# Performance work log

Hardware: AMD Instinct MI355X
Metric: run time of the kernel (lower is better)

## Reference

```python
import jax, jax.numpy as jnp
import numpy as np

B, T, D, H = 64, 1024, 300, 512
Hd = H // 2  # per-direction GRU hidden size


def setup_inputs() -> dict:
    key = jax.random.key(0)
    ks = jax.random.split(key, 12)
    s = 0.05
    return {
        "x": jax.random.normal(ks[0], (B, T, D), jnp.float32),
        "lengths": jax.random.randint(ks[1], (B,), 1, T + 1, jnp.int32),
        # forward-direction GRU params (torch layout: [3*Hd, in])
        "w_ih_f": jax.random.normal(ks[2], (3 * Hd, D), jnp.float32) * s,
        "w_hh_f": jax.random.normal(ks[3], (3 * Hd, Hd), jnp.float32) * s,
        "b_ih_f": jax.random.normal(ks[4], (3 * Hd,), jnp.float32) * s,
        "b_hh_f": jax.random.normal(ks[5], (3 * Hd,), jnp.float32) * s,
        # backward-direction GRU params
        "w_ih_b": jax.random.normal(ks[6], (3 * Hd, D), jnp.float32) * s,
        "w_hh_b": jax.random.normal(ks[7], (3 * Hd, Hd), jnp.float32) * s,
        "b_ih_b": jax.random.normal(ks[8], (3 * Hd,), jnp.float32) * s,
        "b_hh_b": jax.random.normal(ks[9], (3 * Hd,), jnp.float32) * s,
        # attention: hidden layer [H, H] + bias, context vector [H] (no bias)
        "att_w": jax.random.normal(ks[10], (H, H), jnp.float32) * s,
        "att_b": jnp.zeros((H,), jnp.float32),
        "ctx_v": jax.random.normal(ks[11], (H,), jnp.float32) * s,
    }


def _gru_dir(x, w_ih, w_hh, b_ih, b_hh):
    """Single-direction GRU over padded [B,T,D] input, h0=0. Torch gate math."""
    gx = jnp.einsum("btd,gd->btg", x, w_ih) + b_ih  # [B,T,3Hd], big GEMM up front

    def step(h, gx_t):
        gh = h @ w_hh.T + b_hh
        xr, xz, xn = jnp.split(gx_t, 3, axis=-1)
        hr, hz, hn = jnp.split(gh, 3, axis=-1)
        r = jax.nn.sigmoid(xr + hr)
        z = jax.nn.sigmoid(xz + hz)
        n = jnp.tanh(xn + r * hn)
        h = (1.0 - z) * n + z * h
        return h, h

    h0 = jnp.zeros((x.shape[0], w_hh.shape[1]), x.dtype)
    _, hs = jax.lax.scan(step, h0, jnp.swapaxes(gx, 0, 1))  # [T,B,Hd]
    return jnp.swapaxes(hs, 0, 1)  # [B,T,Hd]


def _forward(x, lengths, w_ih_f, w_hh_f, b_ih_f, b_hh_f,
             w_ih_b, w_hh_b, b_ih_b, b_hh_b, att_w, att_b, ctx_v):
    mask = jnp.arange(T)[None, :] < lengths[:, None]  # [B,T]
    xm = x * mask[..., None].astype(x.dtype)  # original pads sequences with 0
    # bidirectional GRU: backward dir runs over the full padded sequence
    # (zeros included), exactly like the original padded nn.GRU call.
    enc_f = _gru_dir(xm, w_ih_f, w_hh_f, b_ih_f, b_hh_f)
    enc_b = _gru_dir(xm[:, ::-1], w_ih_b, w_hh_b, b_ih_b, b_hh_b)[:, ::-1]
    enc = jnp.concatenate([enc_f, enc_b], axis=-1)  # [B,T,H]
    # attention: tanh hidden layer -> context vector -> masked softmax over T
    u = jnp.tanh(jnp.einsum("bth,oh->bto", enc, att_w) + att_b)
    logits = jnp.einsum("bth,h->bt", u, ctx_v)
    logits = jnp.where(mask, logits, -jnp.inf)
    att = jax.nn.softmax(logits, axis=-1)  # pad positions get exact 0 weight
    return jnp.einsum("bt,bth->bh", att, enc)  # weighted sum pooling -> [B,H]


def reference(x, lengths, w_ih_f, w_hh_f, b_ih_f, b_hh_f,
              w_ih_b, w_hh_b, b_ih_b, b_hh_b, att_w, att_b, ctx_v):
    return _forward(x, lengths, w_ih_f, w_hh_f, b_ih_f, b_hh_f,
                    w_ih_b, w_hh_b, b_ih_b, b_hh_b, att_w, att_b, ctx_v)
```

## Files before the change

### kernel.cpp

```cpp
#include <hip/hip_runtime.h>

#define T_SEQ 1024
#define BATCH 64
#define DIN   300
#define DPAD  320
#define HD    256
#define NW    1536
#define ROWS  65536

typedef _Float16 f16x8 __attribute__((ext_vector_type(8)));
typedef _Float16 h2_t  __attribute__((ext_vector_type(2)));
typedef float    f32x4 __attribute__((ext_vector_type(4)));

__device__ __forceinline__ float dot2f(h2_t a, h2_t b, float c) {
#if __has_builtin(__builtin_amdgcn_fdot2)
    return __builtin_amdgcn_fdot2(a, b, c, false);
#else
    return c + (float)a[0]*(float)b[0] + (float)a[1]*(float)b[1];
#endif
}

__device__ __forceinline__ float sigmoidf_(float x) { return 1.f/(1.f+__expf(-x)); }
__device__ __forceinline__ float tanhf_(float x)    { return 1.f - 2.f/(__expf(2.f*x)+1.f); }

__global__ void prep_x(const float* __restrict__ x, const int* __restrict__ len,
                       _Float16* __restrict__ xh) {
    int r = blockIdx.x, k = threadIdx.x;
    int b = r >> 10, t = r & 1023;
    float v = (k < DIN && t < len[b]) ? x[(size_t)r*DIN + k] : 0.f;
    xh[(size_t)r*DPAD + k] = (_Float16)v;
}

__global__ void prep_w(const float* __restrict__ wihf, const float* __restrict__ wihb,
                       const float* __restrict__ bihf, const float* __restrict__ bihb,
                       const float* __restrict__ attw,
                       _Float16* __restrict__ wih, _Float16* __restrict__ attwh,
                       float* __restrict__ bih) {
    int bid = blockIdx.x, tid = threadIdx.x;
    if (bid < NW) {
        const float* src = (bid < 768) ? (wihf + (size_t)bid*DIN)
                                       : (wihb + (size_t)(bid-768)*DIN);
        if (tid < DPAD)
            wih[(size_t)bid*DPAD + tid] = (_Float16)((tid < DIN) ? src[tid] : 0.f);
        if (tid == 0)
            bih[bid] = (bid < 768) ? bihf[bid] : bihb[bid-768];
    } else {
        int n = bid - NW;
        attwh[(size_t)n*512 + tid] = (_Float16)attw[(size_t)n*512 + tid];
    }
}

__global__ __launch_bounds__(256) void gemm_gx(const _Float16* __restrict__ xh,
                                               const _Float16* __restrict__ wih,
                                               const float* __restrict__ bih,
                                               _Float16* __restrict__ gx) {
    int m0 = blockIdx.x * 64, n0 = blockIdx.y * 128;
    __shared__ _Float16 As[64][40];
    __shared__ _Float16 Bs[128][40];
    int tid = threadIdx.x;
    int wave = tid >> 6, lane = tid & 63;
    f32x4 acc[8] = {};
    for (int kt = 0; kt < 10; ++kt) {
        int k0 = kt * 32;
        {
            int r = tid >> 2, ko = (tid & 3) * 8;
            *(f16x8*)&As[r][ko] = *(const f16x8*)&xh[(size_t)(m0+r)*DPAD + k0 + ko];
        }
        {
            int r = tid >> 1, ko = (tid & 1) * 16;
            *(f16x8*)&Bs[r][ko]   = *(const f16x8*)&wih[(size_t)(n0+r)*DPAD + k0 + ko];
            *(f16x8*)&Bs[r][ko+8] = *(const f16x8*)&wih[(size_t)(n0+r)*DPAD + k0 + ko + 8];
        }
        __syncthreads();
        int kk = (lane >> 4) * 8;
        f16x8 a = *(const f16x8*)&As[wave*16 + (lane & 15)][kk];
#pragma unroll
        for (int nf = 0; nf < 8; ++nf) {
            f16x8 bfr = *(const f16x8*)&Bs[nf*16 + (lane & 15)][kk];
            acc[nf] = __builtin_amdgcn_mfma_f32_16x16x32_f16(a, bfr, acc[nf], 0, 0, 0);
        }
        __syncthreads();
    }
#pragma unroll
    for (int nf = 0; nf < 8; ++nf) {
        int n = n0 + nf*16 + (lane & 15);
        float bv = bih[n];
#pragma unroll
        for (int r = 0; r < 4; ++r) {
            int m = m0 + wave*16 + (lane >> 4)*4 + r;
            gx[(size_t)m*NW + n] = (_Float16)(acc[nf][r] + bv);
        }
    }
}

__global__ void __launch_bounds__(512)
__attribute__((amdgpu_waves_per_eu(2, 2)))
gru_kernel(
        const float* __restrict__ whhf, const float* __restrict__ whhb,
        const float* __restrict__ bhhf, const float* __restrict__ bhhb,
        const _Float16* __restrict__ gx, _Float16* __restrict__ enc) {
    int bid = blockIdx.x;
    int dir = bid & 1, b = bid >> 1;
    int tid = threadIdx.x;
    int j = tid >> 1;
    int half = tid & 1;
    const float* whh = dir ? whhb : whhf;
    const float* bhh = dir ? bhhb : bhhf;

    h2_t wr[64], wz[64], wn[64];
    {
        const float2* pr = (const float2*)(whh + (size_t)j*HD        + half*128);
        const float2* pz = (const float2*)(whh + (size_t)(HD + j)*HD + half*128);
        const float2* pn = (const float2*)(whh + (size_t)(2*HD+j)*HD + half*128);
#pragma unroll
        for (int k2 = 0; k2 < 64; ++k2) {
            float2 a = pr[k2]; wr[k2] = h2_t{(_Float16)a.x, (_Float16)a.y};
            float2 c = pz[k2]; wz[k2] = h2_t{(_Float16)c.x, (_Float16)c.y};
            float2 d = pn[k2]; wn[k2] = h2_t{(_Float16)d.x, (_Float16)d.y};
        }
    }
    float brh = half ? 0.f : bhh[j];
    float bzh = half ? 0.f : bhh[HD + j];
    float bnh = half ? 0.f : bhh[2*HD + j];

    __shared__ __align__(16) _Float16 hbuf[2][HD];
    if (tid < HD) hbuf[0][tid] = (_Float16)0.f;
    float hprev = 0.f;
    __syncthreads();

    const _Float16* gxb = gx + (size_t)b*T_SEQ*NW + dir*768 + j;
    int t = dir ? (T_SEQ - 1) : 0;
    int dt = dir ? -1 : 1;
    const _Float16* gp0 = gxb + (size_t)t*NW;
    float xr = (float)gp0[0], xz = (float)gp0[HD], xn = (float)gp0[2*HD];
    int cur = 0;

    for (int s = 0; s < T_SEQ; ++s) {
        float nxr = 0.f, nxz = 0.f, nxn = 0.f;
        if (s + 1 < T_SEQ) {
            const _Float16* gq = gxb + (size_t)(t + dt)*NW;
            nxr = (float)gq[0]; nxz = (float)gq[HD]; nxn = (float)gq[2*HD];
        }

        float hr0 = brh, hz0 = bzh, hn0 = bnh;
        float hr1 = 0.f, hz1 = 0.f, hn1 = 0.f;
        const _Float16* hb = &hbuf[cur][half*128];
#pragma unroll
        for (int k = 0; k < 16; ++k) {
            f16x8 hv = *(const f16x8*)&hb[k*8];
            h2_t a0 = {hv[0], hv[1]}, a1 = {hv[2], hv[3]};
            h2_t a2 = {hv[4], hv[5]}, a3 = {hv[6], hv[7]};
            hr0 = dot2f(a0, wr[4*k+0], hr0); hr1 = dot2f(a1, wr[4*k+1], hr1);
            hr0 = dot2f(a2, wr[4*k+2], hr0); hr1 = dot2f(a3, wr[4*k+3], hr1);
            hz0 = dot2f(a0, wz[4*k+0], hz0); hz1 = dot2f(a1, wz[4*k+1], hz1);
            hz0 = dot2f(a2, wz[4*k+2], hz0); hz1 = dot2f(a3, wz[4*k+3], hz1);
            hn0 = dot2f(a0, wn[4*k+0], hn0); hn1 = dot2f(a1, wn[4*k+1], hn1);
            hn0 = dot2f(a2, wn[4*k+2], hn0); hn1 = dot2f(a3, wn[4*k+3], hn1);
        }
        float hr = hr0 + hr1, hz = hz0 + hz1, hn = hn0 + hn1;
        hr += __shfl_xor(hr, 1);
        hz += __shfl_xor(hz, 1);
        hn += __shfl_xor(hn, 1);

        float r  = sigmoidf_(xr + hr);
        float z  = sigmoidf_(xz + hz);
        float nn = tanhf_(xn + r * hn);
        float h  = (1.f - z) * nn + z * hprev;
        hprev = h;
        float hnb = __shfl_xor(h, 2);
        if (!half)
            enc[((size_t)(b*T_SEQ + t))*512 + dir*HD + j] = (_Float16)h;
        if ((tid & 3) == 0) {
            h2_t hp = {(_Float16)h, (_Float16)hnb};
            *(h2_t*)&hbuf[cur ^ 1][j] = hp;
        }
        __syncthreads();
        xr = nxr; xz = nxz; xn = nxn;
        cur ^= 1; t += dt;
    }
}

__global__ __launch_bounds__(256) void gemm_u(const _Float16* __restrict__ enc,
                                              const _Float16* __restrict__ attwh,
                                              const float* __restrict__ attb,
                                              const float* __restrict__ ctx,
                                              float* __restrict__ logits) {
    int m0 = blockIdx.x * 64;
    __shared__ _Float16 As[64][40];
    __shared__ _Float16 Bs[512][40];
    int tid = threadIdx.x;
    int wave = tid >> 6, lane = tid & 63;
    f32x4 acc[32] = {};
    for (int kt = 0; kt < 16; ++kt) {
        int k0 = kt * 32;
        {
            int r = tid >> 2, ko = (tid & 3) * 8;
            *(f16x8*)&As[r][ko] = *(const f16x8*)&enc[(size_t)(m0+r)*512 + k0 + ko];
        }
        {
#pragma unroll
            for (int jr = 0; jr < 2; ++jr) {
                int row = tid*2 + jr;
#pragma unroll
                for (int q = 0; q < 4; ++q)
                    *(f16x8*)&Bs[row][q*8] =
                        *(const f16x8*)&attwh[(size_t)row*512 + k0 + q*8];
            }
        }
        __syncthreads();
        int kk = (lane >> 4) * 8;
        f16x8 a = *(const f16x8*)&As[wave*16 + (lane & 15)][kk];
#pragma unroll
        for (int nf = 0; nf < 32; ++nf) {
            f16x8 bfr = *(const f16x8*)&Bs[nf*16 + (lane & 15)][kk];
            acc[nf] = __builtin_amdgcn_mfma_f32_16x16x32_f16(a, bfr, acc[nf], 0, 0, 0);
        }
        __syncthreads();
    }
    float rs0 = 0.f, rs1 = 0.f, rs2 = 0.f, rs3 = 0.f;
#pragma unroll
    for (int nf = 0; nf < 32; ++nf) {
        int n = nf*16 + (lane & 15);
        float bv = attb[n], cv = ctx[n];
        rs0 += tanhf_(acc[nf][0] + bv) * cv;
        rs1 += tanhf_(acc[nf][1] + bv) * cv;
        rs2 += tanhf_(acc[nf][2] + bv) * cv;
        rs3 += tanhf_(acc[nf][3] + bv) * cv;
    }
#pragma unroll
    for (int off = 1; off < 16; off <<= 1) {
        rs0 += __shfl_xor(rs0, off);
        rs1 += __shfl_xor(rs1, off);
        rs2 += __shfl_xor(rs2, off);
        rs3 += __shfl_xor(rs3, off);
    }
    if ((lane & 15) == 0) {
        int mb = m0 + wave*16 + (lane >> 4)*4;
        logits[mb + 0] = rs0;
        logits[mb + 1] = rs1;
        logits[mb + 2] = rs2;
        logits[mb + 3] = rs3;
    }
}

__global__ __launch_bounds__(256) void softmax_pool(const float* __restrict__ logits,
                                                    const _Float16* __restrict__ enc,
                                                    const int* __restrict__ lengths,
                                                    float* __restrict__ out) {
    int b = blockIdx.x, tid = threadIdx.x;
    int len = lengths[b];
    if (len < 1) len = 1;
    if (len > T_SEQ) len = T_SEQ;
    __shared__ float att[T_SEQ];
    __shared__ float red[8];
    const float* lg = logits + (size_t)b*T_SEQ;

    float m = -1e30f;
    for (int t = tid; t < len; t += 256) m = fmaxf(m, lg[t]);
#pragma unroll
    for (int off = 1; off < 64; off <<= 1) m = fmaxf(m, __shfl_xor(m, off));
    if ((tid & 63) == 0) red[tid >> 6] = m;
    __syncthreads();
    m = fmaxf(fmaxf(red[0], red[1]), fmaxf(red[2], red[3]));

    float s = 0.f;
    for (int t = tid; t < len; t += 256) {
        float e = __expf(lg[t] - m);
        att[t] = e;
        s += e;
    }
#pragma unroll
    for (int off = 1; off < 64; off <<= 1) s += __shfl_xor(s, off);
    if ((tid & 63) == 0) red[4 + (tid >> 6)] = s;
    __syncthreads();
    s = red[4] + red[5] + red[6] + red[7];
    float inv = 1.f / s;

    float a0 = 0.f, a1 = 0.f;
    const _Float16* eb = enc + (size_t)b*T_SEQ*512;
    for (int t = 0; t < len; ++t) {
        float w = att[t];
        a0 += w * (float)eb[(size_t)t*512 + tid];
        a1 += w * (float)eb[(size_t)t*512 + 256 + tid];
    }
    out[(size_t)b*512 + tid]       = a0 * inv;
    out[(size_t)b*512 + 256 + tid] = a1 * inv;
}

extern "C" void kernel_launch(void* const* d_in, const int* in_sizes, int n_in,
                              void* d_out, int out_size, void* d_ws, size_t ws_size,
                              hipStream_t stream) {
    const float* x    = (const float*)d_in[0];
    const int*   len  = (const int*)  d_in[1];
    const float* wihf = (const float*)d_in[2];
    const float* whhf = (const float*)d_in[3];
    const float* bihf = (const float*)d_in[4];
    const float* bhhf = (const float*)d_in[5];
    const float* wihb = (const float*)d_in[6];
    const float* whhb = (const float*)d_in[7];
    const float* bihb = (const float*)d_in[8];
    const float* bhhb = (const float*)d_in[9];
    const float* attw = (const float*)d_in[10];
    const float* attb = (const float*)d_in[11];
    const float* ctxv = (const float*)d_in[12];
    float* out = (float*)d_out;

    char* ws = (char*)d_ws;
    size_t off = 0;
    _Float16* xh    = (_Float16*)(ws + off); off += (size_t)ROWS*DPAD*2;
    _Float16* wih   = (_Float16*)(ws + off); off += (size_t)NW*DPAD*2;
    _Float16* attwh = (_Float16*)(ws + off); off += (size_t)512*512*2;
    float*    bih   = (float*)   (ws + off); off += (size_t)NW*4;
    _Float16* gx    = (_Float16*)(ws + off); off += (size_t)ROWS*NW*2;
    _Float16* enc   = (_Float16*)(ws + off); off += (size_t)ROWS*512*2;
    float*    logit = (float*)   (ws + off); off += (size_t)ROWS*4;

    prep_x<<<dim3(ROWS), dim3(DPAD), 0, stream>>>(x, len, xh);
    prep_w<<<dim3(NW + 512), dim3(512), 0, stream>>>(wihf, wihb, bihf, bihb, attw,
                                                     wih, attwh, bih);
    gemm_gx<<<dim3(ROWS/64, NW/128), dim3(256), 0, stream>>>(xh, wih, bih, gx);
    gru_kernel<<<dim3(2*BATCH), dim3(512), 0, stream>>>(whhf, whhb, bhhf, bhhb, gx, enc);
    gemm_u<<<dim3(ROWS/64), dim3(256), 0, stream>>>(enc, attwh, attb, ctxv, logit);
    softmax_pool<<<dim3(BATCH), dim3(256), 0, stream>>>(logit, enc, len, out);
}
```

Measured before the change: 1.709 ms.

## Hold z/n recurrent weights in AGPRs and pack encoder output stores

Moves the z and n gate recurrent weight fragments into accumulation registers with inline asm, read back with v_accvgpr_read before each dot2. This relieves VGPR pressure, and the waves_per_eu(2,2) attribute is dropped. The encoder output write is also merged into the same half2 store that updates the shared hidden buffer. The risk is the extra accvgpr_read instructions on the serial per-step critical path.

```diff
diff --git a/kernel.cpp b/kernel.cpp
--- a/kernel.cpp
+++ b/kernel.cpp
@@ -18,6 +18,17 @@
 #else
     return c + (float)a[0]*(float)b[0] + (float)a[1]*(float)b[1];
 #endif
+}
+
+#define AGPR_W(dst, src) \
+    asm volatile("v_accvgpr_write_b32 %0, %1" : "=a"(dst) : "v"(src))
+__device__ __forceinline__ int agpr_r(int a) {
+    int v;
+    asm volatile("v_accvgpr_read_b32 %0, %1" : "=v"(v) : "a"(a));
+    return v;
+}
+__device__ __forceinline__ float dot2a(h2_t h, int wbits, float c) {
+    return dot2f(h, __builtin_bit_cast(h2_t, agpr_r(wbits)), c);
 }
 
 __device__ __forceinline__ float sigmoidf_(float x) { return 1.f/(1.f+__expf(-x)); }
@@ -94,7 +105,6 @@
 }
 
 __global__ void __launch_bounds__(512)
-__attribute__((amdgpu_waves_per_eu(2, 2)))
 gru_kernel(
         const float* __restrict__ whhf, const float* __restrict__ whhb,
         const float* __restrict__ bhhf, const float* __restrict__ bhhb,
@@ -107,16 +117,22 @@
     const float* whh = dir ? whhb : whhf;
     const float* bhh = dir ? bhhb : bhhf;
 
-    h2_t wr[64], wz[64], wn[64];
+    h2_t wr[64];
+    int  wza[64], wna[64];
     {
         const float2* pr = (const float2*)(whh + (size_t)j*HD        + half*128);
         const float2* pz = (const float2*)(whh + (size_t)(HD + j)*HD + half*128);
         const float2* pn = (const float2*)(whh + (size_t)(2*HD+j)*HD + half*128);
 #pragma unroll
-        for (int k2 = 0; k2 < 64; ++k2) {
-            float2 a = pr[k2]; wr[k2] = h2_t{(_Float16)a.x, (_Float16)a.y};
-            float2 c = pz[k2]; wz[k2] = h2_t{(_Float16)c.x, (_Float16)c.y};
-            float2 d = pn[k2]; wn[k2] = h2_t{(_Float16)d.x, (_Float16)d.y};
+        for (int k = 0; k < 64; ++k) {
+            float2 a = pr[k];
+            wr[k] = h2_t{(_Float16)a.x, (_Float16)a.y};
+            float2 c = pz[k];
+            h2_t z2 = h2_t{(_Float16)c.x, (_Float16)c.y};
+            AGPR_W(wza[k], __builtin_bit_cast(int, z2));
+            float2 d = pn[k];
+            h2_t n2 = h2_t{(_Float16)d.x, (_Float16)d.y};
+            AGPR_W(wna[k], __builtin_bit_cast(int, n2));
         }
     }
     float brh = half ? 0.f : bhh[j];
@@ -142,22 +158,22 @@
             nxr = (float)gq[0]; nxz = (float)gq[HD]; nxn = (float)gq[2*HD];
         }
 
-        float hr0 = brh, hz0 = bzh, hn0 = bnh;
-        float hr1 = 0.f, hz1 = 0.f, hn1 = 0.f;
-        const _Float16* hb = &hbuf[cur][half*128];
-#pragma unroll
-        for (int k = 0; k < 16; ++k) {
-            f16x8 hv = *(const f16x8*)&hb[k*8];
+        float ar = brh, az = bzh, an = bnh;
+        float ar1 = 0.f, az1 = 0.f, an1 = 0.f;
+        const _Float16* hseg = &hbuf[cur][half*128];
+#pragma unroll
+        for (int k8 = 0; k8 < 16; ++k8) {
+            f16x8 hv = *(const f16x8*)&hseg[k8*8];
             h2_t a0 = {hv[0], hv[1]}, a1 = {hv[2], hv[3]};
             h2_t a2 = {hv[4], hv[5]}, a3 = {hv[6], hv[7]};
-            hr0 = dot2f(a0, wr[4*k+0], hr0); hr1 = dot2f(a1, wr[4*k+1], hr1);
-            hr0 = dot2f(a2, wr[4*k+2], hr0); hr1 = dot2f(a3, wr[4*k+3], hr1);
-            hz0 = dot2f(a0, wz[4*k+0], hz0); hz1 = dot2f(a1, wz[4*k+1], hz1);
-            hz0 = dot2f(a2, wz[4*k+2], hz0); hz1 = dot2f(a3, wz[4*k+3], hz1);
-            hn0 = dot2f(a0, wn[4*k+0], hn0); hn1 = dot2f(a1, wn[4*k+1], hn1);
-            hn0 = dot2f(a2, wn[4*k+2], hn0); hn1 = dot2f(a3, wn[4*k+3], hn1);
-        }
-        float hr = hr0 + hr1, hz = hz0 + hz1, hn = hn0 + hn1;
+            ar  = dot2f(a0, wr[4*k8+0], ar);  ar1 = dot2f(a1, wr[4*k8+1], ar1);
+            ar  = dot2f(a2, wr[4*k8+2], ar);  ar1 = dot2f(a3, wr[4*k8+3], ar1);
+            az  = dot2a(a0, wza[4*k8+0], az); az1 = dot2a(a1, wza[4*k8+1], az1);
+            az  = dot2a(a2, wza[4*k8+2], az); az1 = dot2a(a3, wza[4*k8+3], az1);
+            an  = dot2a(a0, wna[4*k8+0], an); an1 = dot2a(a1, wna[4*k8+1], an1);
+            an  = dot2a(a2, wna[4*k8+2], an); an1 = dot2a(a3, wna[4*k8+3], an1);
+        }
+        float hr = ar + ar1, hz = az + az1, hn = an + an1;
         hr += __shfl_xor(hr, 1);
         hz += __shfl_xor(hz, 1);
         hn += __shfl_xor(hn, 1);
@@ -167,12 +183,12 @@
         float nn = tanhf_(xn + r * hn);
         float h  = (1.f - z) * nn + z * hprev;
         hprev = h;
-        float hnb = __shfl_xor(h, 2);
-        if (!half)
-            enc[((size_t)(b*T_SEQ + t))*512 + dir*HD + j] = (_Float16)h;
+
+        float hpar = __shfl_xor(h, 2);
         if ((tid & 3) == 0) {
-            h2_t hp = {(_Float16)h, (_Float16)hnb};
+            h2_t hp = {(_Float16)h, (_Float16)hpar};
             *(h2_t*)&hbuf[cur ^ 1][j] = hp;
+            *(h2_t*)&enc[((size_t)(b*T_SEQ + t))*512 + dir*HD + j] = hp;
         }
         __syncthreads();
         xr = nxr; xz = nxz; xn = nxn;
```

New measurement: 2.638 ms. 54.3% more time.
